# Optimization experiments

Measured on AMD Instinct MI355X. Metric: run time of the kernel, lower is better.

## Reference

```python
import jax, jax.numpy as jnp
import numpy as np

EPS = 1e-8

def setup_inputs() -> dict:
    key = jax.random.key(0)
    k1, k2 = jax.random.split(key)
    N, C, S = 2000000, 32, 8
    feats = jax.random.normal(k1, (N, C), dtype=jnp.float32)
    seg_ids = jnp.sort(jax.random.randint(k2, (N,), 0, S, dtype=jnp.int32))
    weight = jnp.ones((1, C), dtype=jnp.float32)
    bias = jnp.zeros((1, C), dtype=jnp.float32)
    return {"feats": feats, "seg_ids": seg_ids, "weight": weight, "bias": bias, "num_segments": S}

def reference(feats, seg_ids, weight, bias, num_segments):
    # Per-instance (segment) mean: GlobalPoolingForward with average=True
    counts = jax.ops.segment_sum(jnp.ones((feats.shape[0], 1), feats.dtype), seg_ids,
                                 num_segments=num_segments)  # [S,1]
    counts = jnp.maximum(counts, 1.0)
    mean = jax.ops.segment_sum(feats, seg_ids, num_segments=num_segments) / counts  # [S,C]
    # BroadcastForward ADDITION with -mean
    centered = feats - mean[seg_ids]  # [N,C]
    # Second global pooling: per-instance variance
    var = jax.ops.segment_sum(centered * centered, seg_ids, num_segments=num_segments) / counts  # [S,C]
    inv_std = jax.lax.rsqrt(var + EPS)  # [S,C]
    # BroadcastForward MULTIPLICATION with inv_std, then affine
    norm = centered * inv_std[seg_ids]
    return norm * weight + bias
```

## Files before the change

kernel.cpp:

```cpp
#include <hip/hip_runtime.h>
#include <math.h>


#define NSH      8
#define SHARD_F  4160
#define WS_SCALE (NSH * SHARD_F)
#define WS_SHIFT (WS_SCALE + 2048)

#define NB    4
#define STEPS 32

typedef float f32x4 __attribute__((ext_vector_type(4)));

typedef const __attribute__((address_space(1))) unsigned int ga_u32;
typedef __attribute__((address_space(3))) unsigned int la_u32;
#define GLL16(gp, lp) \
    __builtin_amdgcn_global_load_lds((ga_u32*)(gp), (la_u32*)(lp), 16, 0, 0)

__global__ __launch_bounds__(256) void zero_ws_kernel(float* __restrict__ ws) {
    int t = blockIdx.x * blockDim.x + threadIdx.x;
    if (t < NSH * SHARD_F) ws[t] = 0.0f;
}

__global__ __launch_bounds__(256) void reduce_kernel(
        const float* __restrict__ feats, const int* __restrict__ seg,
        float* __restrict__ ws, int total4, int N) {
    __shared__ __align__(16) char dma[4 * NB * 1024];
    __shared__ float s_sum[2048];
    __shared__ float s_sq[2048];
    __shared__ float s_cnt[64];
    int t = threadIdx.x;
    for (int j = t; j < 2048; j += 256) { s_sum[j] = 0.0f; s_sq[j] = 0.0f; }
    if (t < 64) s_cnt[t] = 0.0f;
    __syncthreads();

    int wid  = t >> 6;
    int lane = t & 63;
    int cg   = lane & 7;
    const f32x4* f4 = (const f32x4*)feats;
    long ebase = ((long)blockIdx.x * 4 + wid) * 2048;

    if (ebase < total4) {
        long eend = ebase + 2048;
        if (eend > total4) eend = total4;
        int row0 = (int)(ebase >> 3);
        int row1 = (int)((eend - 1) >> 3);
        int sA = seg[row0];
        int sB = seg[row1];
        f32x4 acc  = {0.f, 0.f, 0.f, 0.f};
        f32x4 accq = {0.f, 0.f, 0.f, 0.f};

        if (sA == sB && (eend - ebase) == 2048) {
            const char* g = (const char*)(f4 + ebase) + lane * 16;
            char* lb = &dma[wid * (NB * 1024)];
            asm volatile("s_waitcnt vmcnt(0)" ::: "memory");
            #pragma unroll
            for (int k = 0; k < NB; ++k)
                GLL16(g + k * 1024, lb + k * 1024);
            for (int k = 0; k < STEPS - NB; ++k) {
                asm volatile("s_waitcnt vmcnt(3)" ::: "memory");
                __builtin_amdgcn_sched_barrier(0);
                f32x4 v = *(const f32x4*)(lb + (k & (NB - 1)) * 1024 + lane * 16);
                acc  += v;
                accq += v * v;
                __builtin_amdgcn_sched_barrier(0);
                GLL16(g + (k + NB) * 1024, lb + (k & (NB - 1)) * 1024);
            }
            asm volatile("s_waitcnt vmcnt(0)" ::: "memory");
            __builtin_amdgcn_sched_barrier(0);
            #pragma unroll
            for (int k = STEPS - NB; k < STEPS; ++k) {
                f32x4 v = *(const f32x4*)(lb + (k & (NB - 1)) * 1024 + lane * 16);
                acc  += v;
                accq += v * v;
            }
            #pragma unroll
            for (int m = 8; m <= 32; m <<= 1) {
                acc.x  += __shfl_xor(acc.x, m);  acc.y  += __shfl_xor(acc.y, m);
                acc.z  += __shfl_xor(acc.z, m);  acc.w  += __shfl_xor(acc.w, m);
                accq.x += __shfl_xor(accq.x, m); accq.y += __shfl_xor(accq.y, m);
                accq.z += __shfl_xor(accq.z, m); accq.w += __shfl_xor(accq.w, m);
            }
            if (lane < 8) {
                int bse = sA * 32 + lane * 4;
                atomicAdd(&s_sum[bse + 0], acc.x);
                atomicAdd(&s_sum[bse + 1], acc.y);
                atomicAdd(&s_sum[bse + 2], acc.z);
                atomicAdd(&s_sum[bse + 3], acc.w);
                atomicAdd(&s_sq[bse + 0], accq.x);
                atomicAdd(&s_sq[bse + 1], accq.y);
                atomicAdd(&s_sq[bse + 2], accq.z);
                atomicAdd(&s_sq[bse + 3], accq.w);
            }
            if (lane == 0) atomicAdd(&s_cnt[sA], 256.0f);
        } else {
            for (long e = ebase + lane; e < eend; e += 64) {
                int s = seg[(int)(e >> 3)];
                f32x4 v = f4[e];
                int bse = s * 32 + cg * 4;
                atomicAdd(&s_sum[bse + 0], v.x);
                atomicAdd(&s_sum[bse + 1], v.y);
                atomicAdd(&s_sum[bse + 2], v.z);
                atomicAdd(&s_sum[bse + 3], v.w);
                atomicAdd(&s_sq[bse + 0], v.x * v.x);
                atomicAdd(&s_sq[bse + 1], v.y * v.y);
                atomicAdd(&s_sq[bse + 2], v.z * v.z);
                atomicAdd(&s_sq[bse + 3], v.w * v.w);
                if (cg == 0) atomicAdd(&s_cnt[s], 1.0f);
            }
        }
    }
    __syncthreads();

    float* shard = ws + (blockIdx.x & (NSH - 1)) * SHARD_F;
    for (int j = t; j < 2048; j += 256) {
        float a = s_sum[j];
        float q = s_sq[j];
        if (a != 0.0f) atomicAdd(&shard[j], a);
        if (q != 0.0f) atomicAdd(&shard[2048 + j], q);
    }
    if (t < 64) {
        float c = s_cnt[t];
        if (c != 0.0f) atomicAdd(&shard[4096 + t], c);
    }
}

__global__ void stats_kernel(const float* __restrict__ w,
                             const float* __restrict__ b,
                             const int* __restrict__ nsp,
                             float* __restrict__ ws) {
    int t  = threadIdx.x;
    int ns = min(*nsp, 64);
    for (int o = t; o < ns * 32; o += 256) {
        int s = o >> 5, c = o & 31;
        float S = 0.f, Q = 0.f, C = 0.f;
        #pragma unroll
        for (int sh = 0; sh < NSH; ++sh) {
            const float* base = ws + sh * SHARD_F;
            S += base[o];
            Q += base[2048 + o];
            C += base[4096 + s];
        }
        float cnt  = fmaxf(C, 1.0f);
        float mean = S / cnt;
        float var  = fmaxf(Q / cnt - mean * mean, 0.0f);
        float inv  = rsqrtf(var + 1e-8f);
        float sc   = inv * w[c];
        ws[WS_SCALE + o] = sc;
        ws[WS_SHIFT + o] = b[c] - mean * sc;
    }
}

__global__ __launch_bounds__(256) void apply_kernel(
        const float* __restrict__ feats, const int* __restrict__ seg,
        const float* __restrict__ ws, float* __restrict__ out, int total4) {
    const f32x4* f4 = (const f32x4*)feats;
    f32x4*       o4 = (f32x4*)out;
    const f32x4* scale4 = (const f32x4*)(ws + WS_SCALE);
    const f32x4* shift4 = (const f32x4*)(ws + WS_SHIFT);
    int stride = gridDim.x * blockDim.x;
    for (int i = blockIdx.x * blockDim.x + threadIdx.x; i < total4; i += stride) {
        int row = i >> 3, cg = i & 7;
        int s = seg[row];
        f32x4 v  = f4[i];
        f32x4 sc = scale4[s * 8 + cg];
        f32x4 sh = shift4[s * 8 + cg];
        f32x4 o;
        o.x = fmaf(v.x, sc.x, sh.x); o.y = fmaf(v.y, sc.y, sh.y);
        o.z = fmaf(v.z, sc.z, sh.z); o.w = fmaf(v.w, sc.w, sh.w);
        __builtin_nontemporal_store(o, &o4[i]);
    }
}

extern "C" void kernel_launch(void* const* d_in, const int* in_sizes, int n_in,
                              void* d_out, int out_size, void* d_ws, size_t ws_size,
                              hipStream_t stream) {
    const float* feats = (const float*)d_in[0];
    const int*   seg   = (const int*)d_in[1];
    const float* w     = (const float*)d_in[2];
    const float* b     = (const float*)d_in[3];
    const int*   nsp   = (const int*)d_in[4];
    float* out = (float*)d_out;
    float* ws  = (float*)d_ws;

    int N = in_sizes[1];
    int total4 = N * 8;
    int nwaves = (total4 + 2047) / 2048;
    int nblk_r = (nwaves + 3) / 4;

    hipLaunchKernelGGL(zero_ws_kernel, dim3((NSH * SHARD_F + 255) / 256), dim3(256),
                       0, stream, ws);
    hipLaunchKernelGGL(reduce_kernel, dim3(nblk_r), dim3(256), 0, stream,
                       feats, seg, ws, total4, N);
    hipLaunchKernelGGL(stats_kernel, dim3(1), dim3(256), 0, stream,
                       w, b, nsp, ws);
    hipLaunchKernelGGL(apply_kernel, dim3(4096), dim3(256), 0, stream,
                       feats, seg, ws, out, total4);
}
```

Before: 148.4 us.

## Replace per-block shared histogram with per-wave records and direct flush

Drops the 16KB shared sum/square histograms, their zeroing and the 2048-entry flush loop. Each fast-path wave now writes its 65 partials into a small per-wave record. After one barrier, 65 threads merge the four records and issue one global atomic each, or one per wave when segment ids differ. The slow path at segment boundaries now sends atomics straight to the global shard. The launch bound is raised to request 8 blocks per CU, aiming at higher occupancy from the smaller LDS footprint, at the cost of more global atomic contention on boundary waves.

```diff
diff --git a/kernel.cpp b/kernel.cpp
--- a/kernel.cpp
+++ b/kernel.cpp
@@ -22,106 +22,122 @@
     if (t < NSH * SHARD_F) ws[t] = 0.0f;
 }
 
-__global__ __launch_bounds__(256) void reduce_kernel(
+__global__ __launch_bounds__(256, 8) void reduce_kernel(
         const float* __restrict__ feats, const int* __restrict__ seg,
         float* __restrict__ ws, int total4, int N) {
     __shared__ __align__(16) char dma[4 * NB * 1024];
-    __shared__ float s_sum[2048];
-    __shared__ float s_sq[2048];
-    __shared__ float s_cnt[64];
-    int t = threadIdx.x;
-    for (int j = t; j < 2048; j += 256) { s_sum[j] = 0.0f; s_sq[j] = 0.0f; }
-    if (t < 64) s_cnt[t] = 0.0f;
-    __syncthreads();
-
+    __shared__ float rec[4][68];
+
+    int t    = threadIdx.x;
     int wid  = t >> 6;
     int lane = t & 63;
     int cg   = lane & 7;
     const f32x4* f4 = (const f32x4*)feats;
     long ebase = ((long)blockIdx.x * 4 + wid) * 2048;
-
-    if (ebase < total4) {
-        long eend = ebase + 2048;
-        if (eend > total4) eend = total4;
-        int row0 = (int)(ebase >> 3);
-        int row1 = (int)((eend - 1) >> 3);
-        int sA = seg[row0];
-        int sB = seg[row1];
+    float* shard = ws + (blockIdx.x & (NSH - 1)) * SHARD_F;
+
+    bool active = ebase < total4;
+    long eend = ebase + 2048;
+    if (eend > total4) eend = total4;
+    int sA = 0, sB = 0;
+    bool fastp = false;
+    if (active) {
+        sA = seg[(int)(ebase >> 3)];
+        sB = seg[(int)((eend - 1) >> 3)];
+        fastp = (sA == sB) && ((eend - ebase) == 2048);
+    }
+
+    if (fastp) {
         f32x4 acc  = {0.f, 0.f, 0.f, 0.f};
         f32x4 accq = {0.f, 0.f, 0.f, 0.f};
-
-        if (sA == sB && (eend - ebase) == 2048) {
-            const char* g = (const char*)(f4 + ebase) + lane * 16;
-            char* lb = &dma[wid * (NB * 1024)];
-            asm volatile("s_waitcnt vmcnt(0)" ::: "memory");
-            #pragma unroll
-            for (int k = 0; k < NB; ++k)
-                GLL16(g + k * 1024, lb + k * 1024);
-            for (int k = 0; k < STEPS - NB; ++k) {
-                asm volatile("s_waitcnt vmcnt(3)" ::: "memory");
-                __builtin_amdgcn_sched_barrier(0);
-                f32x4 v = *(const f32x4*)(lb + (k & (NB - 1)) * 1024 + lane * 16);
-                acc  += v;
-                accq += v * v;
-                __builtin_amdgcn_sched_barrier(0);
-                GLL16(g + (k + NB) * 1024, lb + (k & (NB - 1)) * 1024);
-            }
-            asm volatile("s_waitcnt vmcnt(0)" ::: "memory");
+        const char* g = (const char*)(f4 + ebase) + lane * 16;
+        char* lb = &dma[wid * (NB * 1024)];
+        asm volatile("s_waitcnt vmcnt(0)" ::: "memory");
+        #pragma unroll
+        for (int k = 0; k < NB; ++k)
+            GLL16(g + k * 1024, lb + k * 1024);
+        for (int k = 0; k < STEPS - NB; ++k) {
+            asm volatile("s_waitcnt vmcnt(3)" ::: "memory");
             __builtin_amdgcn_sched_barrier(0);
-            #pragma unroll
-            for (int k = STEPS - NB; k < STEPS; ++k) {
-                f32x4 v = *(const f32x4*)(lb + (k & (NB - 1)) * 1024 + lane * 16);
-                acc  += v;
-                accq += v * v;
-            }
-            #pragma unroll
-            for (int m = 8; m <= 32; m <<= 1) {
-                acc.x  += __shfl_xor(acc.x, m);  acc.y  += __shfl_xor(acc.y, m);
-                acc.z  += __shfl_xor(acc.z, m);  acc.w  += __shfl_xor(acc.w, m);
-                accq.x += __shfl_xor(accq.x, m); accq.y += __shfl_xor(accq.y, m);
-                accq.z += __shfl_xor(accq.z, m); accq.w += __shfl_xor(accq.w, m);
-            }
-            if (lane < 8) {
-                int bse = sA * 32 + lane * 4;
-                atomicAdd(&s_sum[bse + 0], acc.x);
-                atomicAdd(&s_sum[bse + 1], acc.y);
-                atomicAdd(&s_sum[bse + 2], acc.z);
-                atomicAdd(&s_sum[bse + 3], acc.w);
-                atomicAdd(&s_sq[bse + 0], accq.x);
-                atomicAdd(&s_sq[bse + 1], accq.y);
-                atomicAdd(&s_sq[bse + 2], accq.z);
-                atomicAdd(&s_sq[bse + 3], accq.w);
-            }
-            if (lane == 0) atomicAdd(&s_cnt[sA], 256.0f);
-        } else {
+            f32x4 v = *(const f32x4*)(lb + (k & (NB - 1)) * 1024 + lane * 16);
+            acc  += v;
+            accq += v * v;
+            __builtin_amdgcn_sched_barrier(0);
+            GLL16(g + (k + NB) * 1024, lb + (k & (NB - 1)) * 1024);
+        }
+        asm volatile("s_waitcnt vmcnt(0)" ::: "memory");
+        __builtin_amdgcn_sched_barrier(0);
+        #pragma unroll
+        for (int k = STEPS - NB; k < STEPS; ++k) {
+            f32x4 v = *(const f32x4*)(lb + (k & (NB - 1)) * 1024 + lane * 16);
+            acc  += v;
+            accq += v * v;
+        }
+        #pragma unroll
+        for (int m = 8; m <= 32; m <<= 1) {
+            acc.x  += __shfl_xor(acc.x, m);  acc.y  += __shfl_xor(acc.y, m);
+            acc.z  += __shfl_xor(acc.z, m);  acc.w  += __shfl_xor(acc.w, m);
+            accq.x += __shfl_xor(accq.x, m); accq.y += __shfl_xor(accq.y, m);
+            accq.z += __shfl_xor(accq.z, m); accq.w += __shfl_xor(accq.w, m);
+        }
+        if (lane < 8) {
+            rec[wid][lane * 4 + 0]      = acc.x;
+            rec[wid][lane * 4 + 1]      = acc.y;
+            rec[wid][lane * 4 + 2]      = acc.z;
+            rec[wid][lane * 4 + 3]      = acc.w;
+            rec[wid][32 + lane * 4 + 0] = accq.x;
+            rec[wid][32 + lane * 4 + 1] = accq.y;
+            rec[wid][32 + lane * 4 + 2] = accq.z;
+            rec[wid][32 + lane * 4 + 3] = accq.w;
+        }
+        if (lane == 0) {
+            rec[wid][64] = 256.0f;
+            rec[wid][65] = (float)sA;
+        }
+    } else {
+        if (lane == 0) rec[wid][65] = -1.0f;
+        if (active) {
             for (long e = ebase + lane; e < eend; e += 64) {
                 int s = seg[(int)(e >> 3)];
                 f32x4 v = f4[e];
                 int bse = s * 32 + cg * 4;
-                atomicAdd(&s_sum[bse + 0], v.x);
-                atomicAdd(&s_sum[bse + 1], v.y);
-                atomicAdd(&s_sum[bse + 2], v.z);
-                atomicAdd(&s_sum[bse + 3], v.w);
-                atomicAdd(&s_sq[bse + 0], v.x * v.x);
-                atomicAdd(&s_sq[bse + 1], v.y * v.y);
-                atomicAdd(&s_sq[bse + 2], v.z * v.z);
-                atomicAdd(&s_sq[bse + 3], v.w * v.w);
-                if (cg == 0) atomicAdd(&s_cnt[s], 1.0f);
+                atomicAdd(&shard[bse + 0], v.x);
+                atomicAdd(&shard[bse + 1], v.y);
+                atomicAdd(&shard[bse + 2], v.z);
+                atomicAdd(&shard[bse + 3], v.w);
+                atomicAdd(&shard[2048 + bse + 0], v.x * v.x);
+                atomicAdd(&shard[2048 + bse + 1], v.y * v.y);
+                atomicAdd(&shard[2048 + bse + 2], v.z * v.z);
+                atomicAdd(&shard[2048 + bse + 3], v.w * v.w);
+                if (cg == 0) atomicAdd(&shard[4096 + s], 1.0f);
             }
         }
     }
     __syncthreads();
 
-    float* shard = ws + (blockIdx.x & (NSH - 1)) * SHARD_F;
-    for (int j = t; j < 2048; j += 256) {
-        float a = s_sum[j];
-        float q = s_sq[j];
-        if (a != 0.0f) atomicAdd(&shard[j], a);
-        if (q != 0.0f) atomicAdd(&shard[2048 + j], q);
-    }
-    if (t < 64) {
-        float c = s_cnt[t];
-        if (c != 0.0f) atomicAdd(&shard[4096 + t], c);
+    if (t < 65) {
+        float s0 = rec[0][65], s1 = rec[1][65], s2 = rec[2][65], s3 = rec[3][65];
+        bool allsame = (s0 >= 0.0f) && (s0 == s1) && (s1 == s2) && (s2 == s3);
+        if (allsame) {
+            float v = rec[0][t] + rec[1][t] + rec[2][t] + rec[3][t];
+            int s = (int)s0;
+            float* dst = (t < 32)  ? &shard[s * 32 + t]
+                       : (t < 64)  ? &shard[2048 + s * 32 + (t - 32)]
+                                   : &shard[4096 + s];
+            atomicAdd(dst, v);
+        } else {
+            #pragma unroll
+            for (int r = 0; r < 4; ++r) {
+                float sid = rec[r][65];
+                if (sid >= 0.0f) {
+                    int s = (int)sid;
+                    float* dst = (t < 32)  ? &shard[s * 32 + t]
+                               : (t < 64)  ? &shard[2048 + s * 32 + (t - 32)]
+                                           : &shard[4096 + s];
+                    atomicAdd(dst, rec[r][t]);
+                }
+            }
+        }
     }
 }
 
```

New measurement: 143.6 us. -3.2%, faster.
